# Optimization experiments

Hardware: AMD Instinct MI355X
Metric: run time of the kernel (lower is better)

## Reference

```python
import jax, jax.numpy as jnp
import numpy as np

B, S, V, HD, HID, ND = 32, 32, 100, 32, 64, 10


def setup_inputs() -> dict:
    key = jax.random.key(0)
    ks = jax.random.split(key, 32)
    gaps = jax.random.uniform(ks[0], (B, S), jnp.float32) * 0.1 + 0.01
    batch_train_time = jnp.cumsum(gaps, axis=1)                      # sorted event times
    batch_train_type = jax.random.randint(ks[1], (B, S), 0, V)       # event marks in [0, V)
    batch_train_mask = jnp.ones((B, S), jnp.float32)

    def lin(k, i, o):
        return jax.random.normal(k, (i, o), jnp.float32) * (1.0 / np.sqrt(i))

    inp = dict(batch_train_time=batch_train_time,
               batch_train_type=batch_train_type,
               batch_train_mask=batch_train_mask,
               logits=jnp.zeros((2, V * V), jnp.float32),            # torch init: zeros
               h0=jax.random.normal(ks[2], (V, HD), jnp.float32) * 0.01,
               # drift f: in = h_dim + diff_t + last_t
               fW1=lin(ks[3], HD + 2, HID), fb1=jnp.zeros((HID,)),
               fW2=lin(ks[4], HID, HID), fb2=jnp.zeros((HID,)),
               fW3=lin(ks[5], HID, HD), fb3=jnp.zeros((HD,)),
               # diffusion g: in = h_dim + diff_t
               gW1=lin(ks[6], HD + 1, HID), gb1=jnp.zeros((HID,)),
               gW2=lin(ks[7], HID, HID), gb2=jnp.zeros((HID,)),
               gW3=lin(ks[8], HID, HD), gb3=jnp.zeros((HD,)),
               # intensity e: h -> softplus scalar per vertex
               eW1=lin(ks[9], HD, HID), eb1=jnp.zeros((HID,)),
               eW2=lin(ks[10], HID, 1), eb2=jnp.zeros((1,)),
               # jump h
               jW1=lin(ks[11], HD, HID), jb1=jnp.zeros((HID,)),
               jW2=lin(ks[12], HID, HD), jb2=jnp.zeros((HD,)),
               # A_MSG edge mlp: [h_send, h_recv] -> message
               mW1=lin(ks[13], 2 * HD, HID), mb1=jnp.zeros((HID,)),
               mW2=lin(ks[14], HID, HD), mb2=jnp.zeros((HD,)))
    return inp


def reference(batch_train_time, batch_train_type, batch_train_mask, logits, h0,
              fW1, fb1, fW2, fb2, fW3, fb3,
              gW1, gb1, gW2, gb2, gW3, gb3,
              eW1, eb1, eW2, eb2, jW1, jb1, jW2, jb2, mW1, mb1, mW2, mb2):
    barange = jnp.arange(B)
    edge_prob = jax.nn.softmax(logits, axis=0)[1]  # [V*V], P(edge present)

    def mlp3(x, W1, b1, W2, b2, W3, b3):
        h = jnp.tanh(x @ W1 + b1)
        h = jnp.tanh(h @ W2 + b2)
        return h @ W3 + b3

    def f_drift(h, dft, last):
        return mlp3(jnp.concatenate([h, dft, last], -1), fW1, fb1, fW2, fb2, fW3, fb3)

    def g_diff(h, dft):
        return mlp3(jnp.concatenate([h, dft], -1), gW1, gb1, gW2, gb2, gW3, gb3)

    def e_int(h):  # [B,V,HD] -> [B,V] positive intensity
        return jax.nn.softplus(jnp.tanh(h @ eW1 + eb1) @ eW2 + eb2)[..., 0]

    def jump(h):
        return jnp.tanh(h @ jW1 + jb1) @ jW2 + jb2

    def msg_jump(h, ev):
        # message passing from the event node to every vertex, gated by edge_prob
        send = h[barange, ev]                                          # [B,HD]
        pair = jnp.concatenate([jnp.broadcast_to(send[:, None, :], h.shape), h], -1)
        m = jnp.tanh(pair @ mW1 + mb1) @ mW2 + mb2                     # [B,V,HD]
        p = edge_prob[ev[:, None] * V + jnp.arange(V)[None, :]]        # [B,V]
        h = h + m * p[:, :, None]
        # jump update at the event node
        he = h[barange, ev]
        return h.at[barange, ev].add(jump(he))

    def euler(h, t0, t1, key):
        dt = (t1 - t0) / ND                                            # [B]
        dtb = dt[:, None, None]
        l_init = e_int(h)

        def step(carry, j):
            h, k = carry
            k, sub = jax.random.split(k)
            noise = jax.random.normal(sub, h.shape, h.dtype)
            dft = jnp.broadcast_to(dtb * (j + 1.0), (B, V, 1))
            last = jnp.broadcast_to(t0[:, None, None], (B, V, 1))
            h = h + f_drift(h, dft, last) * dtb + g_diff(h, dft) * jnp.sqrt(dtb) * noise
            return (h, k), e_int(h)

        (h, key), ls = jax.lax.scan(step, (h, key), jnp.arange(ND, dtype=jnp.float32))
        l_ts = jnp.concatenate([l_init[:, :, None], jnp.moveaxis(ls, 0, 2)], axis=2)  # [B,V,ND+1]
        ts = t0[:, None] + dt[:, None] * jnp.arange(ND + 1, dtype=dt.dtype)           # [B,ND+1]
        return h, key, ts, l_ts

    # t = 0: initial intensity + first jump
    h = jnp.broadcast_to(h0[None], (B, V, HD))
    l0 = e_int(h)
    ev0 = batch_train_type[:, 0]
    lt0 = l0[barange, ev0]
    h = msg_jump(h, ev0)
    key = jax.random.key(42)

    def interval(carry, xs):
        h, key = carry
        t0, t1, ev = xs
        h, key, ts, l_ts = euler(h, t0, t1, key)
        l_last = l_ts[:, :, -1]                 # pre-jump (left) intensities
        lt = l_last[barange, ev]
        h = msg_jump(h, ev)
        return (h, key), (ts, l_ts, l_last, lt)

    xs = (batch_train_time[:, :-1].T, batch_train_time[:, 1:].T, batch_train_type[:, 1:].T)
    (_h, _k), (ts_all, lts_all, llast_all, lt_all) = jax.lax.scan(interval, (h, key), xs)

    tsave = jnp.moveaxis(ts_all, 0, 1).reshape(B, -1)                       # [B,(S-1)*(ND+1)]
    a_l_tsave = jnp.transpose(lts_all, (1, 2, 0, 3)).reshape(B, V, -1)      # [B,V,(S-1)*(ND+1)]
    a_l_batch_l = jnp.concatenate([l0[:, None, :], jnp.moveaxis(llast_all, 0, 1)], axis=1)  # [B,S,V]
    a_l_time_l = jnp.concatenate([lt0[:, None], lt_all.T], axis=1)          # [B,S]

    sum_term = jnp.sum(jnp.log(a_l_time_l + 1e-16) * batch_train_mask)
    em = jnp.repeat(batch_train_mask[:, 1:], ND + 1, axis=1)                # [B,(S-1)*(ND+1)]
    em = jnp.broadcast_to(em[:, None, :], a_l_tsave.shape)
    lts = a_l_tsave * em
    dts = jnp.diff(tsave, axis=1)[:, None, :]
    integral = jnp.sum((lts[:, :, :-1] * em[:, :, :-1] + lts[:, :, 1:] * em[:, :, 1:])
                       * (dts * em[:, :, 1:])) / 2
    a_nll = integral - sum_term
    return a_nll, a_l_batch_l
```

## Files before the change

### kernel.cpp

```cpp
#include <hip/hip_runtime.h>
#include <hip/hip_fp16.h>
#include <stdint.h>

#define B_  32
#define S_  32
#define V_  100
#define HD_ 32
#define HID_ 64
#define ND_ 10
#define NROW (B_*V_)
#define NTILE 7
#define NBLK (B_*NTILE)

#define WO_WB    0
#define WO_HA    9728
#define WO_HB    (WO_HA + NROW*HD_)
#define WO_ACC   (WO_HB + NROW*HD_)
#define WO_PREVL (WO_ACC + NROW)
#define WO_PREVT (WO_PREVL + NROW)
#define WO_LTLOG (WO_PREVT + NROW)
#define WO_END   (WO_LTLOG + B_*S_)
#define NOISE_FLOATS ((size_t)310 * NBLK * 64 * 8)

typedef __attribute__((ext_vector_type(8))) _Float16 f16x8;
typedef __attribute__((ext_vector_type(4))) float f32x4;

#define LGKM_FENCE asm volatile("s_waitcnt lgkmcnt(0)" ::: "memory")

__host__ __device__ inline void tf2x32(uint32_t k0, uint32_t k1,
                                       uint32_t& x0, uint32_t& x1) {
  uint32_t ks0 = k0, ks1 = k1, ks2 = k0 ^ k1 ^ 0x1BD11BDAu;
#define TFR(r) { x0 += x1; x1 = (x1 << (r)) | (x1 >> (32 - (r))); x1 ^= x0; }
  x0 += ks0; x1 += ks1;
  TFR(13) TFR(15) TFR(26) TFR(6)
  x0 += ks1; x1 += ks2 + 1u;
  TFR(17) TFR(29) TFR(16) TFR(24)
  x0 += ks2; x1 += ks0 + 2u;
  TFR(13) TFR(15) TFR(26) TFR(6)
  x0 += ks0; x1 += ks1 + 3u;
  TFR(17) TFR(29) TFR(16) TFR(24)
  x0 += ks1; x1 += ks2 + 4u;
  TFR(13) TFR(15) TFR(26) TFR(6)
  x0 += ks2; x1 += ks0 + 5u;
#undef TFR
}

__device__ __forceinline__ float erfinv_f(float x) {
  float w = -log1pf(-x * x);
  float p;
  if (w < 5.0f) {
    w -= 2.5f;
    p = 2.81022636e-08f;
    p = fmaf(p, w, 3.43273939e-07f);
    p = fmaf(p, w, -3.5233877e-06f);
    p = fmaf(p, w, -4.39150654e-06f);
    p = fmaf(p, w, 0.00021858087f);
    p = fmaf(p, w, -0.00125372503f);
    p = fmaf(p, w, -0.00417768164f);
    p = fmaf(p, w, 0.246640727f);
    p = fmaf(p, w, 1.50140941f);
  } else {
    w = sqrtf(w) - 3.0f;
    p = -0.000200214257f;
    p = fmaf(p, w, 0.000100950558f);
    p = fmaf(p, w, 0.00134934322f);
    p = fmaf(p, w, -0.00367342844f);
    p = fmaf(p, w, 0.00573950773f);
    p = fmaf(p, w, -0.0076224613f);
    p = fmaf(p, w, 0.00943887047f);
    p = fmaf(p, w, 1.00167406f);
    p = fmaf(p, w, 2.83297682f);
  }
  return p * x;
}

__device__ __forceinline__ float tanh_e(float x) {
  float e = __builtin_amdgcn_exp2f(x * 2.885390082f);
  return 1.0f - 2.0f * __builtin_amdgcn_rcpf(e + 1.0f);
}
__device__ __forceinline__ float softplus_fast(float x) {
  return fmaxf(x, 0.0f) + __logf(1.0f + __expf(-fabsf(x)));
}
__device__ __forceinline__ unsigned short f16b(float x) {
  __half h = __float2half(x);
  return *reinterpret_cast<unsigned short*>(&h);
}
__device__ __forceinline__ f32x4 MF(f16x8 a, f16x8 b, f32x4 c) {
  return __builtin_amdgcn_mfma_f32_16x16x32_f16(a, b, c, 0, 0, 0);
}

struct SubK { uint32_t k[ND_][2]; };
struct AllK { uint32_t k[310][2]; };

__device__ __forceinline__ void noise8(int row0, int lane, uint32_t k0, uint32_t k1,
                                       float* n) {
  int g = lane >> 4, li = lane & 15;
#pragma unroll
  for (int v = 0; v < 8; ++v) {
    int reg = v & 3, t = v >> 2;
    int row = row0 + 4 * g + reg;
    uint32_t x0 = 0u, x1 = (uint32_t)(row * HD_ + li + 16 * t);
    tf2x32(k0, k1, x0, x1);
    uint32_t bits = x0 ^ x1;
    float fr = __uint_as_float(0x3f800000u | (bits >> 9)) - 1.0f;
    const float LOW = -0.99999994f;
    float u = fmaxf(LOW, fr * 2.0f + LOW);
    n[v] = 1.4142135f * erfinv_f(u);
  }
}

__global__ void prep_k(const float* __restrict__ fW1, const float* __restrict__ gW1,
                       const float* __restrict__ fW2, const float* __restrict__ gW2,
                       const float* __restrict__ fW3, const float* __restrict__ gW3,
                       const float* __restrict__ eW1, const float* __restrict__ eW2,
                       unsigned short* __restrict__ wb) {
  int tid = blockIdx.x * 256 + threadIdx.x;
  if (tid >= 38 * 64) return;
  int fid = tid >> 6, lane = tid & 63;
  int g = lane >> 4, li = lane & 15;
  const float* src; int k0 = 0, n0 = 0, ncol = HID_; bool hperm = false, col0 = false;
  if (fid < 4)       { src = fW1; n0 = 16 * fid;       hperm = true; }
  else if (fid < 8)  { src = gW1; n0 = 16 * (fid - 4); hperm = true; }
  else if (fid < 16) { int q = fid - 8;  src = fW2; n0 = 16 * (q >> 1); k0 = 32 * (q & 1); }
  else if (fid < 24) { int q = fid - 16; src = gW2; n0 = 16 * (q >> 1); k0 = 32 * (q & 1); }
  else if (fid < 28) { int q = fid - 24; src = fW3; n0 = 16 * (q >> 1); k0 = 32 * (q & 1); ncol = HD_; }
  else if (fid < 32) { int q = fid - 28; src = gW3; n0 = 16 * (q >> 1); k0 = 32 * (q & 1); ncol = HD_; }
  else if (fid < 36) { src = eW1; n0 = 16 * (fid - 32); hperm = true; }
  else               { src = eW2; k0 = 32 * (fid - 36); col0 = true; }
  unsigned short v[8];
#pragma unroll
  for (int j = 0; j < 8; ++j) {
    int s = k0 + 8 * g + j;
    int k = hperm ? ((s >> 1) + 16 * (s & 1)) : ((s >> 2) + 16 * (s & 3));
    float x;
    if (col0) x = (li == 0) ? src[k] : 0.0f;
    else      x = src[k * ncol + (n0 + li)];
    v[j] = f16b(x);
  }
  uint4 o;
  o.x = (uint32_t)v[0] | ((uint32_t)v[1] << 16);
  o.y = (uint32_t)v[2] | ((uint32_t)v[3] << 16);
  o.z = (uint32_t)v[4] | ((uint32_t)v[5] << 16);
  o.w = (uint32_t)v[6] | ((uint32_t)v[7] << 16);
  ((uint4*)wb)[fid * 64 + lane] = o;
}

__global__ void noise_k(float* __restrict__ np, AllK ak) {
  int pair = blockIdx.x * 4 + (threadIdx.x >> 6);
  int lane = threadIdx.x & 63;
  int sg = pair / NBLK, bid = pair - sg * NBLK;
  int b = bid / NTILE, tile = bid - b * NTILE;
  int row0 = b * V_ + tile * 16;
  float n[8];
  noise8(row0, lane, ak.k[sg][0], ak.k[sg][1], n);
  float* dst = np + ((size_t)pair * 64 + lane) * 8;
  f32x4 a = {n[0], n[1], n[2], n[3]}, c = {n[4], n[5], n[6], n[7]};
  ((f32x4*)dst)[0] = a;
  ((f32x4*)dst)[1] = c;
}

__launch_bounds__(64, 1)
__global__ void euler_k(const float* __restrict__ time_, const int* __restrict__ type_,
                        const float* __restrict__ mask_, const float* __restrict__ wsf,
                        const float* __restrict__ fb1, const float* __restrict__ fb2,
                        const float* __restrict__ fb3, const float* __restrict__ gb1,
                        const float* __restrict__ gb2, const float* __restrict__ gb3,
                        const float* __restrict__ eb1, const float* __restrict__ eb2,
                        const float* __restrict__ fW1, const float* __restrict__ gW1,
                        float* __restrict__ h, float* __restrict__ acc,
                        float* __restrict__ prevl, float* __restrict__ prevt,
                        float* __restrict__ ltlog, float* __restrict__ dout,
                        const float* __restrict__ noisep, int s, SubK sk) {
  __shared__ unsigned short actF[16 * 72];
  __shared__ unsigned short actG[16 * 72];
  __shared__ unsigned short hTl[16 * 40];
  __shared__ f16x8 wl[14 * 64];

  const int lane = threadIdx.x;
  const int g = lane >> 4, li = lane & 15;
  const int bid = blockIdx.x;
  const int b = bid / NTILE, tile = bid - b * NTILE;
  const int row0 = b * V_ + tile * 16;
  const int rmax = b * V_ + (V_ - 1);

  const f16x8* WBv = (const f16x8*)wsf;
#pragma unroll
  for (int i = 0; i < 8; ++i) wl[i * 64 + lane] = WBv[i * 64 + lane];
#pragma unroll
  for (int i = 0; i < 4; ++i) wl[(8 + i) * 64 + lane] = WBv[(32 + i) * 64 + lane];
#pragma unroll
  for (int i = 0; i < 2; ++i) wl[(12 + i) * 64 + lane] = WBv[(36 + i) * 64 + lane];

  f16x8 w2f[8], w2g[8], w3f[4], w3g[4];
#pragma unroll
  for (int i = 0; i < 8; ++i) w2f[i] = WBv[(8 + i) * 64 + lane];
#pragma unroll
  for (int i = 0; i < 8; ++i) w2g[i] = WBv[(16 + i) * 64 + lane];
#pragma unroll
  for (int i = 0; i < 4; ++i) w3f[i] = WBv[(24 + i) * 64 + lane];
#pragma unroll
  for (int i = 0; i < 4; ++i) w3g[i] = WBv[(28 + i) * 64 + lane];

  float fb1v[4], gb1v[4], fb2v[4], gb2v[4], eb1v[4], fw32[4], fw33[4], gw32[4];
#pragma unroll
  for (int nt = 0; nt < 4; ++nt) {
    int n = li + 16 * nt;
    fb1v[nt] = fb1[n]; gb1v[nt] = gb1[n];
    fb2v[nt] = fb2[n]; gb2v[nt] = gb2[n];
    eb1v[nt] = eb1[n];
    fw32[nt] = fW1[32 * HID_ + n]; fw33[nt] = fW1[33 * HID_ + n];
    gw32[nt] = gW1[32 * HID_ + n];
  }
  float fb3v[2], gb3v[2];
#pragma unroll
  for (int nt = 0; nt < 2; ++nt) { fb3v[nt] = fb3[li + 16 * nt]; gb3v[nt] = gb3[li + 16 * nt]; }
  const float eb2v = eb2[0];

  const float t0 = time_[b * S_ + s - 1], t1 = time_[b * S_ + s];
  const float dt = (t1 - t0) / 10.0f;
  const float sq = sqrtf(dt);
  const float msk = mask_[b * S_ + s], mskp = mask_[b * S_ + s - 1];

  float hv[2][4];
#pragma unroll
  for (int t = 0; t < 2; ++t)
#pragma unroll
    for (int reg = 0; reg < 4; ++reg) {
      int rv = row0 + 4 * g + reg; if (rv > rmax) rv = rmax;
      hv[t][reg] = h[rv * HD_ + li + 16 * t];
    }
#pragma unroll
  for (int reg = 0; reg < 4; ++reg) {
    uint32_t u = (uint32_t)f16b(hv[0][reg]) | ((uint32_t)f16b(hv[1][reg]) << 16);
    *(uint32_t*)&hTl[(4 * g + reg) * 40 + 2 * li] = u;
  }
  LGKM_FENCE;

  float accv[4], lprev[4];
#pragma unroll
  for (int reg = 0; reg < 4; ++reg) {
    int rv = row0 + 4 * g + reg; if (rv > rmax) rv = rmax;
    accv[reg] = acc[rv];
  }

  auto echain = [&](float* lout) {
    f16x8 ahe = *(const f16x8*)&hTl[li * 40 + 8 * g];
    f32x4 ce[4];
#pragma unroll
    for (int nt = 0; nt < 4; ++nt) {
      f32x4 c = {eb1v[nt], eb1v[nt], eb1v[nt], eb1v[nt]};
      ce[nt] = MF(ahe, wl[(8 + nt) * 64 + lane], c);
    }
#pragma unroll
    for (int reg = 0; reg < 4; ++reg) {
      uint32_t lo = (uint32_t)f16b(tanh_e(ce[0][reg])) | ((uint32_t)f16b(tanh_e(ce[1][reg])) << 16);
      uint32_t hi = (uint32_t)f16b(tanh_e(ce[2][reg])) | ((uint32_t)f16b(tanh_e(ce[3][reg])) << 16);
      uint2 tmp; tmp.x = lo; tmp.y = hi;
      *(uint2*)&actF[(4 * g + reg) * 72 + 4 * li] = tmp;
    }
    LGKM_FENCE;
    f16x8 ae0 = *(const f16x8*)&actF[li * 72 + 8 * g];
    f16x8 ae1 = *(const f16x8*)&actF[li * 72 + 32 + 8 * g];
    f32x4 c2 = {eb2v, eb2v, eb2v, eb2v};
    c2 = MF(ae0, wl[12 * 64 + lane], c2);
    c2 = MF(ae1, wl[13 * 64 + lane], c2);
#pragma unroll
    for (int reg = 0; reg < 4; ++reg) lout[reg] = softplus_fast(c2[reg]);
  };

  echain(lprev);
  if (s > 1) {
#pragma unroll
    for (int reg = 0; reg < 4; ++reg) {
      int rv = row0 + 4 * g + reg; if (rv > rmax) rv = rmax;
      accv[reg] += (prevl[rv] * mskp + lprev[reg] * msk) * (t0 - prevt[rv]) * msk;
    }
  }

#pragma unroll 1
  for (int j = 0; j < ND_; ++j) {
    const float dft = dt * (float)(j + 1);
    float nz[8];
    if (noisep) {
      const float* q = noisep + (((size_t)((s - 1) * ND_ + j) * NBLK + bid) * 64 + lane) * 8;
      f32x4 q0 = ((const f32x4*)q)[0], q1 = ((const f32x4*)q)[1];
      nz[0] = q0[0]; nz[1] = q0[1]; nz[2] = q0[2]; nz[3] = q0[3];
      nz[4] = q1[0]; nz[5] = q1[1]; nz[6] = q1[2]; nz[7] = q1[3];
    } else {
      noise8(row0, lane, sk.k[j][0], sk.k[j][1], nz);
    }

    f16x8 ah = *(const f16x8*)&hTl[li * 40 + 8 * g];
    f32x4 cf[4], cg[4];
#pragma unroll
    for (int nt = 0; nt < 4; ++nt) {
      f32x4 c = {fb1v[nt], fb1v[nt], fb1v[nt], fb1v[nt]};
      cf[nt] = MF(ah, wl[nt * 64 + lane], c);
      f32x4 d = {gb1v[nt], gb1v[nt], gb1v[nt], gb1v[nt]};
      cg[nt] = MF(ah, wl[(4 + nt) * 64 + lane], d);
    }
    float addf[4], addg[4];
#pragma unroll
    for (int nt = 0; nt < 4; ++nt) {
      addf[nt] = dft * fw32[nt] + t0 * fw33[nt];
      addg[nt] = dft * gw32[nt];
    }
#pragma unroll
    for (int reg = 0; reg < 4; ++reg) {
      uint32_t lo = (uint32_t)f16b(tanh_e(cf[0][reg] + addf[0])) | ((uint32_t)f16b(tanh_e(cf[1][reg] + addf[1])) << 16);
      uint32_t hi = (uint32_t)f16b(tanh_e(cf[2][reg] + addf[2])) | ((uint32_t)f16b(tanh_e(cf[3][reg] + addf[3])) << 16);
      uint2 t1v; t1v.x = lo; t1v.y = hi;
      *(uint2*)&actF[(4 * g + reg) * 72 + 4 * li] = t1v;
      uint32_t lo2 = (uint32_t)f16b(tanh_e(cg[0][reg] + addg[0])) | ((uint32_t)f16b(tanh_e(cg[1][reg] + addg[1])) << 16);
      uint32_t hi2 = (uint32_t)f16b(tanh_e(cg[2][reg] + addg[2])) | ((uint32_t)f16b(tanh_e(cg[3][reg] + addg[3])) << 16);
      uint2 t2v; t2v.x = lo2; t2v.y = hi2;
      *(uint2*)&actG[(4 * g + reg) * 72 + 4 * li] = t2v;
    }
    LGKM_FENCE;
    f16x8 af0 = *(const f16x8*)&actF[li * 72 + 8 * g];
    f16x8 af1 = *(const f16x8*)&actF[li * 72 + 32 + 8 * g];
    f16x8 ag0 = *(const f16x8*)&actG[li * 72 + 8 * g];
    f16x8 ag1 = *(const f16x8*)&actG[li * 72 + 32 + 8 * g];
#pragma unroll
    for (int nt = 0; nt < 4; ++nt) {
      f32x4 c = {fb2v[nt], fb2v[nt], fb2v[nt], fb2v[nt]};
      c = MF(af0, w2f[2 * nt], c);
      cf[nt] = MF(af1, w2f[2 * nt + 1], c);
      f32x4 d = {gb2v[nt], gb2v[nt], gb2v[nt], gb2v[nt]};
      d = MF(ag0, w2g[2 * nt], d);
      cg[nt] = MF(ag1, w2g[2 * nt + 1], d);
    }
#pragma unroll
    for (int reg = 0; reg < 4; ++reg) {
      uint32_t lo = (uint32_t)f16b(tanh_e(cf[0][reg])) | ((uint32_t)f16b(tanh_e(cf[1][reg])) << 16);
      uint32_t hi = (uint32_t)f16b(tanh_e(cf[2][reg])) | ((uint32_t)f16b(tanh_e(cf[3][reg])) << 16);
      uint2 t1v; t1v.x = lo; t1v.y = hi;
      *(uint2*)&actF[(4 * g + reg) * 72 + 4 * li] = t1v;
      uint32_t lo2 = (uint32_t)f16b(tanh_e(cg[0][reg])) | ((uint32_t)f16b(tanh_e(cg[1][reg])) << 16);
      uint32_t hi2 = (uint32_t)f16b(tanh_e(cg[2][reg])) | ((uint32_t)f16b(tanh_e(cg[3][reg])) << 16);
      uint2 t2v; t2v.x = lo2; t2v.y = hi2;
      *(uint2*)&actG[(4 * g + reg) * 72 + 4 * li] = t2v;
    }
    LGKM_FENCE;
    af0 = *(const f16x8*)&actF[li * 72 + 8 * g];
    af1 = *(const f16x8*)&actF[li * 72 + 32 + 8 * g];
    ag0 = *(const f16x8*)&actG[li * 72 + 8 * g];
    ag1 = *(const f16x8*)&actG[li * 72 + 32 + 8 * g];
    f32x4 dr[2], di[2];
#pragma unroll
    for (int nt = 0; nt < 2; ++nt) {
      f32x4 c = {fb3v[nt], fb3v[nt], fb3v[nt], fb3v[nt]};
      c = MF(af0, w3f[2 * nt], c);
      dr[nt] = MF(af1, w3f[2 * nt + 1], c);
      f32x4 d = {gb3v[nt], gb3v[nt], gb3v[nt], gb3v[nt]};
      d = MF(ag0, w3g[2 * nt], d);
      di[nt] = MF(ag1, w3g[2 * nt + 1], d);
    }
#pragma unroll
    for (int t = 0; t < 2; ++t)
#pragma unroll
      for (int reg = 0; reg < 4; ++reg)
        hv[t][reg] += dr[t][reg] * dt + di[t][reg] * sq * nz[t * 4 + reg];
#pragma unroll
    for (int reg = 0; reg < 4; ++reg) {
      uint32_t u = (uint32_t)f16b(hv[0][reg]) | ((uint32_t)f16b(hv[1][reg]) << 16);
      *(uint32_t*)&hTl[(4 * g + reg) * 40 + 2 * li] = u;
    }
    LGKM_FENCE;
    float l[4];
    echain(l);
    float tj = t0 + dt * (float)j, tj1 = t0 + dt * (float)(j + 1);
    float dtm = (tj1 - tj) * msk;
#pragma unroll
    for (int reg = 0; reg < 4; ++reg) {
      accv[reg] += (lprev[reg] * msk + l[reg] * msk) * dtm;
      lprev[reg] = l[reg];
    }
  }

#pragma unroll
  for (int t = 0; t < 2; ++t)
#pragma unroll
    for (int reg = 0; reg < 4; ++reg) {
      int v = tile * 16 + 4 * g + reg;
      if (v < V_) h[(row0 + 4 * g + reg) * HD_ + li + 16 * t] = hv[t][reg];
    }
  if (li == 0) {
    int ev = type_[b * S_ + s];
    float pt = t0 + dt * 10.0f;
#pragma unroll
    for (int reg = 0; reg < 4; ++reg) {
      int v = tile * 16 + 4 * g + reg;
      if (v < V_) {
        int rv = row0 + 4 * g + reg;
        acc[rv] = accv[reg];
        prevl[rv] = lprev[reg];
        prevt[rv] = pt;
        dout[1 + (b * S_ + s) * V_ + v] = lprev[reg];
        if (v == ev) ltlog[s * B_ + b] = logf(lprev[reg] + 1e-16f) * msk;
      }
    }
  }
}

template<int K4, int O>
__device__ __forceinline__ float dotWxT(const float* __restrict__ W,
                                        const float* __restrict__ x,
                                        float a, int lane) {
#pragma unroll
  for (int kb = 0; kb < K4; ++kb) {
    float4 xv = *(const float4*)(x + kb * 4);
    a = fmaf(xv.x, W[(kb * 4 + 0) * O + lane], a);
    a = fmaf(xv.y, W[(kb * 4 + 1) * O + lane], a);
    a = fmaf(xv.z, W[(kb * 4 + 2) * O + lane], a);
    a = fmaf(xv.w, W[(kb * 4 + 3) * O + lane], a);
  }
  return a;
}

__launch_bounds__(256)
__global__ void msg_k(const int* __restrict__ type_, const float* __restrict__ mask_,
                      const float* __restrict__ logits, const float* __restrict__ h0,
                      const float* __restrict__ mW1, const float* __restrict__ mb1,
                      const float* __restrict__ mW2, const float* __restrict__ mb2,
                      const float* __restrict__ jW1, const float* __restrict__ jb1,
                      const float* __restrict__ jW2, const float* __restrict__ jb2,
                      const float* __restrict__ eW1, const float* __restrict__ eb1,
                      const float* __restrict__ eW2, const float* __restrict__ eb2,
                      const float* __restrict__ hsrc, float* __restrict__ hdst,
                      float* __restrict__ acc, float* __restrict__ ltlog,
                      float* __restrict__ dout, int s) {
  __shared__ float xls[4][64];
  __shared__ float als[4][64];
  const int w = threadIdx.x >> 6, lane = threadIdx.x & 63;
  const int row = blockIdx.x * 4 + w;
  const int b = row / V_, v = row % V_;
  const int ev = type_[b * S_ + s];

  if (s == 0) {
    const float eb1r = eb1[lane], eW2r = eW2[lane], eb2r = eb2[0];
    if (lane < 32) xls[w][lane] = h0[v * HD_ + lane];
    float a = dotWxT<8, 64>(eW1, xls[w], eb1r, lane);
    float t = tanhf(a) * eW2r;
#pragma unroll
    for (int o = 1; o < 64; o <<= 1) t += __shfl_xor(t, o, 64);
    float l0 = fmaxf(t + eb2r, 0.0f) + log1pf(expf(-fabsf(t + eb2r)));
    if (lane == 0) {
      dout[1 + (b * S_ + 0) * V_ + v] = l0;
      acc[row] = 0.0f;
      if (v == ev) ltlog[0 * B_ + b] = logf(l0 + 1e-16f) * mask_[b * S_ + 0];
    }
  }

  const float mb1r = mb1[lane], jb1r = jb1[lane];
  const float mb2r = (lane < 32) ? mb2[lane] : 0.0f;
  const float jb2r = (lane < 32) ? jb2[lane] : 0.0f;

  if (lane < 32) {
    xls[w][lane]      = (s == 0) ? h0[ev * HD_ + lane] : hsrc[(b * V_ + ev) * HD_ + lane];
    xls[w][32 + lane] = (s == 0) ? h0[v * HD_ + lane]  : hsrc[row * HD_ + lane];
  }
  float a = dotWxT<16, 64>(mW1, xls[w], mb1r, lane);
  als[w][lane] = tanhf(a);

  float p;
  {
    int idx = ev * V_ + v;
    float l0v = logits[idx], l1v = logits[V_ * V_ + idx];
    float mx = fmaxf(l0v, l1v);
    float e0 = expf(l0v - mx), e1 = expf(l1v - mx);
    p = e1 / (e0 + e1);
  }
  float hn = 0.0f;
  if (lane < 32) {
    float mj = dotWxT<16, 32>(mW2, als[w], mb2r, lane);
    hn = xls[w][32 + lane] + mj * p;
  }
  if (v == ev) {
    if (lane < 32) xls[w][lane] = hn;
    float aj = dotWxT<8, 64>(jW1, xls[w], jb1r, lane);
    als[w][lane] = tanhf(aj);
    if (lane < 32) {
      float jj = dotWxT<16, 32>(jW2, als[w], jb2r, lane);
      hn += jj;
    }
  }
  if (lane < 32) hdst[row * HD_ + lane] = hn;
}

__global__ void reduce_k(const float* __restrict__ acc, const float* __restrict__ ltlog,
                         float* __restrict__ dout) {
  __shared__ double sh[512];
  int t = threadIdx.x;
  double ia = 0.0, st = 0.0;
  for (int i = t; i < NROW; i += 256) ia += (double)acc[i];
  for (int i = t; i < B_ * S_; i += 256) st += (double)ltlog[i];
  sh[t] = ia; sh[256 + t] = st;
  __syncthreads();
  for (int o = 128; o > 0; o >>= 1) {
    if (t < o) { sh[t] += sh[t + o]; sh[256 + t] += sh[256 + t + o]; }
    __syncthreads();
  }
  if (t == 0) dout[0] = (float)(0.5 * sh[0] - sh[256]);
}

extern "C" void kernel_launch(void* const* d_in, const int* in_sizes, int n_in,
                              void* d_out, int out_size, void* d_ws, size_t ws_size,
                              hipStream_t stream) {
  const float* time_  = (const float*)d_in[0];
  const int*   type_  = (const int*)d_in[1];
  const float* mask_  = (const float*)d_in[2];
  const float* logits = (const float*)d_in[3];
  const float* h0     = (const float*)d_in[4];
  const float* fW1 = (const float*)d_in[5];  const float* fb1 = (const float*)d_in[6];
  const float* fW2 = (const float*)d_in[7];  const float* fb2 = (const float*)d_in[8];
  const float* fW3 = (const float*)d_in[9];  const float* fb3 = (const float*)d_in[10];
  const float* gW1 = (const float*)d_in[11]; const float* gb1 = (const float*)d_in[12];
  const float* gW2 = (const float*)d_in[13]; const float* gb2 = (const float*)d_in[14];
  const float* gW3 = (const float*)d_in[15]; const float* gb3 = (const float*)d_in[16];
  const float* eW1 = (const float*)d_in[17]; const float* eb1 = (const float*)d_in[18];
  const float* eW2 = (const float*)d_in[19]; const float* eb2 = (const float*)d_in[20];
  const float* jW1 = (const float*)d_in[21]; const float* jb1 = (const float*)d_in[22];
  const float* jW2 = (const float*)d_in[23]; const float* jb2 = (const float*)d_in[24];
  const float* mW1 = (const float*)d_in[25]; const float* mb1 = (const float*)d_in[26];
  const float* mW2 = (const float*)d_in[27]; const float* mb2 = (const float*)d_in[28];
  float* out = (float*)d_out;

  float* ws    = (float*)d_ws;
  float* hA    = ws + WO_HA;
  float* hB    = ws + WO_HB;
  float* acc   = ws + WO_ACC;
  float* prevl = ws + WO_PREVL;
  float* prevt = ws + WO_PREVT;
  float* ltlog = ws + WO_LTLOG;

  uint32_t kh = 0u, kl = 42u;
  uint32_t subs[310][2];
  for (int n = 0; n < 310; ++n) {
    uint32_t a0 = 0u, a1 = 0u; tf2x32(kh, kl, a0, a1);
    uint32_t b0 = 0u, b1 = 1u; tf2x32(kh, kl, b0, b1);
    subs[n][0] = b0; subs[n][1] = b1;
    kh = a0; kl = a1;
  }

  const bool useNoise = ws_size >= ((size_t)WO_END + NOISE_FLOATS) * 4;
  float* noisep = useNoise ? (ws + WO_END) : nullptr;

  prep_k<<<10, 256, 0, stream>>>(fW1, gW1, fW2, gW2, fW3, gW3, eW1, eW2,
                                 (unsigned short*)ws);
  if (useNoise) {
    AllK ak;
    for (int n = 0; n < 310; ++n) { ak.k[n][0] = subs[n][0]; ak.k[n][1] = subs[n][1]; }
    noise_k<<<(310 * NBLK) / 4, 256, 0, stream>>>(noisep, ak);
  }

  dim3 mgrid(NROW / 4), mblk(256);
  msg_k<<<mgrid, mblk, 0, stream>>>(type_, mask_, logits, h0,
                                    mW1, mb1, mW2, mb2, jW1, jb1, jW2, jb2,
                                    eW1, eb1, eW2, eb2,
                                    hA, hA, acc, ltlog, out, 0);
  for (int s = 1; s <= 31; ++s) {
    float* hcur = ((s - 1) & 1) ? hB : hA;
    SubK sk;
    for (int j = 0; j < ND_; ++j) {
      sk.k[j][0] = subs[(s - 1) * ND_ + j][0];
      sk.k[j][1] = subs[(s - 1) * ND_ + j][1];
    }
    euler_k<<<NBLK, 64, 0, stream>>>(time_, type_, mask_, ws,
                                     fb1, fb2, fb3, gb1, gb2, gb3, eb1, eb2,
                                     fW1, gW1,
                                     hcur, acc, prevl, prevt, ltlog, out,
                                     noisep, s, sk);
    if (s < 31) {
      float* hdst = (s & 1) ? hB : hA;
      msg_k<<<mgrid, mblk, 0, stream>>>(type_, mask_, logits, h0,
                                        mW1, mb1, mW2, mb2, jW1, jb1, jW2, jb2,
                                        eW1, eb1, eW2, eb2,
                                        hcur, hdst, acc, ltlog, out, s);
    }
  }
  reduce_k<<<1, 256, 0, stream>>>(acc, ltlog, out);
}
```

Measured before the change: 1.238 ms.

## Generate next interval's noise in a helper wavefront inside the Euler kernel

Replaces the upfront kernel that precomputed noise for all 310 substeps with a double-buffered scheme. Only the first interval's noise is produced beforehand. Each euler_k launch gets a second 64-thread wavefront that computes the next interval's noise into the alternate buffer while the first wavefront integrates. This removes the large precompute pass and its memory footprint, at the cost of an extra wavefront per block.

```diff
diff --git a/kernel.cpp b/kernel.cpp
--- a/kernel.cpp
+++ b/kernel.cpp
@@ -19,8 +19,8 @@
 #define WO_PREVL (WO_ACC + NROW)
 #define WO_PREVT (WO_PREVL + NROW)
 #define WO_LTLOG (WO_PREVT + NROW)
-#define WO_END   (WO_LTLOG + B_*S_)
-#define NOISE_FLOATS ((size_t)310 * NBLK * 64 * 8)
+#define WO_NOISE (WO_LTLOG + B_*S_)
+#define SLICE_F  ((size_t)10 * NBLK * 64 * 8)
 
 typedef __attribute__((ext_vector_type(8))) _Float16 f16x8;
 typedef __attribute__((ext_vector_type(4))) float f32x4;
@@ -90,7 +90,6 @@
 }
 
 struct SubK { uint32_t k[ND_][2]; };
-struct AllK { uint32_t k[310][2]; };
 
 __device__ __forceinline__ void noise8(int row0, int lane, uint32_t k0, uint32_t k1,
                                        float* n) {
@@ -145,21 +144,20 @@
   ((uint4*)wb)[fid * 64 + lane] = o;
 }
 
-__global__ void noise_k(float* __restrict__ np, AllK ak) {
-  int pair = blockIdx.x * 4 + (threadIdx.x >> 6);
-  int lane = threadIdx.x & 63;
-  int sg = pair / NBLK, bid = pair - sg * NBLK;
+__global__ void noise1_k(float* __restrict__ np, SubK sk) {
+  int bid = blockIdx.x, lane = threadIdx.x;
   int b = bid / NTILE, tile = bid - b * NTILE;
   int row0 = b * V_ + tile * 16;
-  float n[8];
-  noise8(row0, lane, ak.k[sg][0], ak.k[sg][1], n);
-  float* dst = np + ((size_t)pair * 64 + lane) * 8;
-  f32x4 a = {n[0], n[1], n[2], n[3]}, c = {n[4], n[5], n[6], n[7]};
-  ((f32x4*)dst)[0] = a;
-  ((f32x4*)dst)[1] = c;
-}
-
-__launch_bounds__(64, 1)
+  for (int j = 0; j < ND_; ++j) {
+    float n[8];
+    noise8(row0, lane, sk.k[j][0], sk.k[j][1], n);
+    float* dst = np + ((size_t)(j * NBLK + bid) * 64 + lane) * 8;
+    f32x4 a = {n[0], n[1], n[2], n[3]}, c = {n[4], n[5], n[6], n[7]};
+    ((f32x4*)dst)[0] = a; ((f32x4*)dst)[1] = c;
+  }
+}
+
+__launch_bounds__(128, 1)
 __global__ void euler_k(const float* __restrict__ time_, const int* __restrict__ type_,
                         const float* __restrict__ mask_, const float* __restrict__ wsf,
                         const float* __restrict__ fb1, const float* __restrict__ fb2,
@@ -170,17 +168,34 @@
                         float* __restrict__ h, float* __restrict__ acc,
                         float* __restrict__ prevl, float* __restrict__ prevt,
                         float* __restrict__ ltlog, float* __restrict__ dout,
-                        const float* __restrict__ noisep, int s, SubK sk) {
+                        const float* __restrict__ nin, float* __restrict__ nout,
+                        int s, SubK skc, SubK skh) {
   __shared__ unsigned short actF[16 * 72];
   __shared__ unsigned short actG[16 * 72];
   __shared__ unsigned short hTl[16 * 40];
   __shared__ f16x8 wl[14 * 64];
 
-  const int lane = threadIdx.x;
-  const int g = lane >> 4, li = lane & 15;
   const int bid = blockIdx.x;
   const int b = bid / NTILE, tile = bid - b * NTILE;
   const int row0 = b * V_ + tile * 16;
+
+  if (threadIdx.x >= 64) {
+    if (nout) {
+      int lane = threadIdx.x - 64;
+#pragma unroll 1
+      for (int j = 0; j < ND_; ++j) {
+        float n[8];
+        noise8(row0, lane, skh.k[j][0], skh.k[j][1], n);
+        float* dst = nout + ((size_t)(j * NBLK + bid) * 64 + lane) * 8;
+        f32x4 a = {n[0], n[1], n[2], n[3]}, c = {n[4], n[5], n[6], n[7]};
+        ((f32x4*)dst)[0] = a; ((f32x4*)dst)[1] = c;
+      }
+    }
+    return;
+  }
+
+  const int lane = threadIdx.x;
+  const int g = lane >> 4, li = lane & 15;
   const int rmax = b * V_ + (V_ - 1);
 
   const f16x8* WBv = (const f16x8*)wsf;
@@ -281,13 +296,13 @@
   for (int j = 0; j < ND_; ++j) {
     const float dft = dt * (float)(j + 1);
     float nz[8];
-    if (noisep) {
-      const float* q = noisep + (((size_t)((s - 1) * ND_ + j) * NBLK + bid) * 64 + lane) * 8;
+    if (nin) {
+      const float* q = nin + ((size_t)(j * NBLK + bid) * 64 + lane) * 8;
       f32x4 q0 = ((const f32x4*)q)[0], q1 = ((const f32x4*)q)[1];
       nz[0] = q0[0]; nz[1] = q0[1]; nz[2] = q0[2]; nz[3] = q0[3];
       nz[4] = q1[0]; nz[5] = q1[1]; nz[6] = q1[2]; nz[7] = q1[3];
     } else {
-      noise8(row0, lane, sk.k[j][0], sk.k[j][1], nz);
+      noise8(row0, lane, skc.k[j][0], skc.k[j][1], nz);
     }
 
     f16x8 ah = *(const f16x8*)&hTl[li * 40 + 8 * g];
@@ -357,10 +372,10 @@
       di[nt] = MF(ag1, w3g[2 * nt + 1], d);
     }
 #pragma unroll
-    for (int t = 0; t < 2; ++t)
-#pragma unroll
-      for (int reg = 0; reg < 4; ++reg)
-        hv[t][reg] += dr[t][reg] * dt + di[t][reg] * sq * nz[t * 4 + reg];
+    for (int reg = 0; reg < 4; ++reg) {
+      hv[0][reg] += dr[0][reg] * dt + di[0][reg] * sq * nz[reg];
+      hv[1][reg] += dr[1][reg] * dt + di[1][reg] * sq * nz[4 + reg];
+    }
 #pragma unroll
     for (int reg = 0; reg < 4; ++reg) {
       uint32_t u = (uint32_t)f16b(hv[0][reg]) | ((uint32_t)f16b(hv[1][reg]) << 16);
@@ -369,7 +384,8 @@
     LGKM_FENCE;
     float l[4];
     echain(l);
-    float tj = t0 + dt * (float)j, tj1 = t0 + dt * (float)(j + 1);
+    float tj  = t0 + dt * (float)j;
+    float tj1 = t0 + dt * (float)(j + 1);
     float dtm = (tj1 - tj) * msk;
 #pragma unroll
     for (int reg = 0; reg < 4; ++reg) {
@@ -543,15 +559,16 @@
     kh = a0; kl = a1;
   }
 
-  const bool useNoise = ws_size >= ((size_t)WO_END + NOISE_FLOATS) * 4;
-  float* noisep = useNoise ? (ws + WO_END) : nullptr;
+  const bool useNoise = ws_size >= ((size_t)WO_NOISE + 2 * SLICE_F) * 4;
+  float* n0 = useNoise ? (ws + WO_NOISE) : nullptr;
+  float* n1 = useNoise ? (ws + WO_NOISE + SLICE_F) : nullptr;
 
   prep_k<<<10, 256, 0, stream>>>(fW1, gW1, fW2, gW2, fW3, gW3, eW1, eW2,
                                  (unsigned short*)ws);
   if (useNoise) {
-    AllK ak;
-    for (int n = 0; n < 310; ++n) { ak.k[n][0] = subs[n][0]; ak.k[n][1] = subs[n][1]; }
-    noise_k<<<(310 * NBLK) / 4, 256, 0, stream>>>(noisep, ak);
+    SubK sk0;
+    for (int j = 0; j < ND_; ++j) { sk0.k[j][0] = subs[j][0]; sk0.k[j][1] = subs[j][1]; }
+    noise1_k<<<NBLK, 64, 0, stream>>>(n1, sk0);
   }
 
   dim3 mgrid(NROW / 4), mblk(256);
@@ -561,16 +578,20 @@
                                     hA, hA, acc, ltlog, out, 0);
   for (int s = 1; s <= 31; ++s) {
     float* hcur = ((s - 1) & 1) ? hB : hA;
-    SubK sk;
+    SubK skc, skh;
     for (int j = 0; j < ND_; ++j) {
-      sk.k[j][0] = subs[(s - 1) * ND_ + j][0];
-      sk.k[j][1] = subs[(s - 1) * ND_ + j][1];
-    }
-    euler_k<<<NBLK, 64, 0, stream>>>(time_, type_, mask_, ws,
-                                     fb1, fb2, fb3, gb1, gb2, gb3, eb1, eb2,
-                                     fW1, gW1,
-                                     hcur, acc, prevl, prevt, ltlog, out,
-                                     noisep, s, sk);
+      skc.k[j][0] = subs[(s - 1) * ND_ + j][0];
+      skc.k[j][1] = subs[(s - 1) * ND_ + j][1];
+      skh.k[j][0] = (s < 31) ? subs[s * ND_ + j][0] : 0u;
+      skh.k[j][1] = (s < 31) ? subs[s * ND_ + j][1] : 0u;
+    }
+    const float* nin = useNoise ? ((s & 1) ? n1 : n0) : nullptr;
+    float* nout = (useNoise && s < 31) ? (((s + 1) & 1) ? n1 : n0) : nullptr;
+    euler_k<<<NBLK, 128, 0, stream>>>(time_, type_, mask_, ws,
+                                      fb1, fb2, fb3, gb1, gb2, gb3, eb1, eb2,
+                                      fW1, gW1,
+                                      hcur, acc, prevl, prevt, ltlog, out,
+                                      nin, nout, s, skc, skh);
     if (s < 31) {
       float* hdst = (s & 1) ? hB : hA;
       msg_k<<<mgrid, mblk, 0, stream>>>(type_, mask_, logits, h0,
```

Measured after the change: 1.315 ms. 6.2% more time.
